# Performance work log

Measured on AMD Instinct MI355X. Metric: run time of the kernel, lower is better.

## Reference

```python
import jax, jax.numpy as jnp
import numpy as np

NUM_HEADS = 8  # from init_kwargs
SR = 2         # sr_ratio from init_kwargs


def layernorm(t, g, b, eps=1e-5):
    mu = jnp.mean(t, axis=-1, keepdims=True)
    var = jnp.mean((t - mu) ** 2, axis=-1, keepdims=True)
    return (t - mu) * jax.lax.rsqrt(var + eps) * g + b


def setup_inputs() -> dict:
    key = jax.random.key(0)
    ks = jax.random.split(key, 6)
    B, C = 4, 256
    Hx = Wx = 64
    Hz = Wz = 32
    N = Hz * Wz + Hx * Wx  # 5120 (template tokens first, then search tokens)
    s = 0.02
    return {
        "x": jax.random.normal(ks[0], (B, N, C), jnp.float32),
        "Wq": jax.random.normal(ks[1], (C, C), jnp.float32) * s,          # nn.Linear(dim, dim, bias=False)
        "Wkv": jax.random.normal(ks[2], (2 * C, C), jnp.float32) * s,     # nn.Linear(dim, 2*dim, bias=False)
        "Wsr": jax.random.normal(ks[3], (C, C, SR, SR), jnp.float32) * s, # Conv2d(dim, dim, k=sr, stride=sr) OIHW
        "bsr": jnp.zeros((C,), jnp.float32),
        "gamma": jnp.ones((C,), jnp.float32),
        "beta": jnp.zeros((C,), jnp.float32),
        "Wproj": jax.random.normal(ks[4], (C, C), jnp.float32) * s,
        "bproj": jnp.zeros((C,), jnp.float32),
        "H_x": Hx, "W_x": Wx, "H_z": Hz, "W_z": Wz,
    }


def reference(x, Wq, Wkv, Wsr, bsr, gamma, beta, Wproj, bproj, H_x, W_x, H_z, W_z):
    B, N, C = x.shape
    h = NUM_HEADS
    d = C // h
    scale = d ** -0.5
    Nz, Nx = H_z * W_z, H_x * W_x

    # q for all tokens: [B, h, N, d]
    q = (x @ Wq.T).reshape(B, N, h, d).transpose(0, 2, 1, 3)

    # spatial reduction (sr_ratio > 1 branch): strided conv + layernorm on each stream
    z_tok, x_tok = x[:, :Nz], x[:, Nz:]
    ker = jnp.transpose(Wsr, (2, 3, 1, 0))  # OIHW -> HWIO

    def sr_branch(t, H, W):
        img = t.reshape(B, H, W, C)  # NHWC; same layout as torch NCHW reshape
        out = jax.lax.conv_general_dilated(
            img, ker, window_strides=(SR, SR), padding="VALID",
            dimension_numbers=("NHWC", "HWIO", "NHWC")) + bsr
        out = out.reshape(B, -1, C)
        return layernorm(out, gamma, beta)

    x_ = sr_branch(x_tok, H_x, W_x)  # [B, (Hx/sr)*(Wx/sr), C]
    z_ = sr_branch(z_tok, H_z, W_z)  # [B, (Hz/sr)*(Wz/sr), C]
    zL = z_.shape[1]
    cat = jnp.concatenate([z_, x_], axis=1)  # [B, L, C]

    kv = (cat @ Wkv.T).reshape(B, -1, 2, h, d).transpose(2, 0, 3, 1, 4)  # [2, B, h, L, d]
    k, v = kv[0], kv[1]

    q_z, q_x = q[:, :, :Nz], q[:, :, Nz:]
    k_z, v_z = k[:, :, :zL], v[:, :, :zL]

    # template queries attend only to reduced template keys/values
    attn_z = jax.nn.softmax(jnp.einsum("bhqd,bhkd->bhqk", q_z, k_z) * scale, axis=-1)
    out_z = jnp.einsum("bhqk,bhkd->bhqd", attn_z, v_z).transpose(0, 2, 1, 3).reshape(B, Nz, C)

    # search queries attend to full (template+search) reduced keys/values
    attn_x = jax.nn.softmax(jnp.einsum("bhqd,bhkd->bhqk", q_x, k) * scale, axis=-1)
    out_x = jnp.einsum("bhqk,bhkd->bhqd", attn_x, v).transpose(0, 2, 1, 3).reshape(B, Nx, C)

    out = jnp.concatenate([out_z, out_x], axis=1)
    return out @ Wproj.T + bproj
```

## Files before the change

kernel.cpp:

```cpp
#include <hip/hip_runtime.h>
#include <hip/hip_bf16.h>
#include <cstddef>

#define BATCH 4
#define CCH 256
#define NHEAD 8
#define DHEAD 32
#define NZ 1024
#define NX 4096
#define NTOK 5120
#define LKV 1280
#define QC 0.25503486f

typedef __attribute__((ext_vector_type(8))) short bf16x8;
typedef __attribute__((ext_vector_type(4))) float floatx4;

__device__ inline short f2bf(float f) {
  __hip_bfloat16 h = __float2bfloat16(f);
  return __builtin_bit_cast(short, h);
}
__device__ inline unsigned int pk2(float a, float b) {
  unsigned int lo = (unsigned short)f2bf(a);
  unsigned int hi = (unsigned short)f2bf(b);
  return lo | (hi << 16);
}
__device__ inline unsigned int pk2f(float a, float b) {
  unsigned int ua = __builtin_bit_cast(unsigned int, a) + 0x8000u;
  unsigned int ub = __builtin_bit_cast(unsigned int, b) + 0x8000u;
  return __builtin_amdgcn_perm(ub, ua, 0x07060302u);
}
__device__ inline void cvt8(const float* __restrict__ src, short* __restrict__ dst, int i) {
  float4 v0 = ((const float4*)src)[i * 2];
  float4 v1 = ((const float4*)src)[i * 2 + 1];
  uint4 u;
  u.x = pk2(v0.x, v0.y); u.y = pk2(v0.z, v0.w);
  u.z = pk2(v1.x, v1.y); u.w = pk2(v1.z, v1.w);
  ((uint4*)dst)[i] = u;
}

__global__ __launch_bounds__(256) void prep_weights(const float* __restrict__ Wq,
                                                    const float* __restrict__ Wkv,
                                                    const float* __restrict__ Wproj,
                                                    const float* __restrict__ Wsr,
                                                    const float* __restrict__ x,
                                                    short* __restrict__ Wqb,
                                                    short* __restrict__ Wkvb,
                                                    short* __restrict__ Wprojb,
                                                    short* __restrict__ Wkb,
                                                    short* __restrict__ xb) {
  int blk = blockIdx.x, tid = threadIdx.x;
  if (blk < 32) {
    cvt8(Wq, Wqb, blk * 256 + tid);
  } else if (blk < 96) {
    cvt8(Wkv, Wkvb, (blk - 32) * 256 + tid);
  } else if (blk < 128) {
    cvt8(Wproj, Wprojb, (blk - 96) * 256 + tid);
  } else if (blk < 1152) {
    int i = (blk - 128) * 256 + tid;
    int co = i >> 10;
    int rem = i & 1023;
    int di = rem >> 9, dj = (rem >> 8) & 1, ci = rem & 255;
    Wkb[i] = f2bf(Wsr[((co * 256 + ci) * 2 + di) * 2 + dj]);
  } else {
    cvt8(x, xb, (blk - 1152) * 256 + tid);
  }
}

#define G64_DECL()                                                           \
  __shared__ short As[64][72];                                               \
  __shared__ short Bs[64][72];                                               \
  int tid = threadIdx.x;                                                     \
  int wave = tid >> 6, lg = (tid & 63) >> 4, lr = tid & 15;                  \
  int sr = tid >> 2, sc = tid & 3;                                           \
  floatx4 acc[4] = {{0.f,0.f,0.f,0.f},{0.f,0.f,0.f,0.f},                     \
                    {0.f,0.f,0.f,0.f},{0.f,0.f,0.f,0.f}};

#define G64_MFMA8()                                                          \
    __syncthreads();                                                         \
    {                                                                        \
      bf16x8 af0 = *(bf16x8*)&As[wave * 16 + lr][lg * 8];                    \
      bf16x8 af1 = *(bf16x8*)&As[wave * 16 + lr][32 + lg * 8];               \
      _Pragma("unroll") for (int n = 0; n < 4; ++n) {                        \
        bf16x8 bf0 = *(bf16x8*)&Bs[n * 16 + lr][lg * 8];                     \
        bf16x8 bf1 = *(bf16x8*)&Bs[n * 16 + lr][32 + lg * 8];                \
        acc[n] = __builtin_amdgcn_mfma_f32_16x16x32_bf16(af0, bf0, acc[n], 0, 0, 0); \
        acc[n] = __builtin_amdgcn_mfma_f32_16x16x32_bf16(af1, bf1, acc[n], 0, 0, 0); \
      }                                                                      \
    }

__global__ __launch_bounds__(256) void gemm_qconv(const short* __restrict__ xb,
                                                  const short* __restrict__ Wqb,
                                                  const short* __restrict__ Wkb,
                                                  short* __restrict__ qbf,
                                                  float* __restrict__ cat_pre) {
  G64_DECL()
  int bidx = blockIdx.x;
  if (bidx < 1280) {
    int bm = (bidx >> 2) * 64, bn = (bidx & 3) * 64;
    for (int k0 = 0; k0 < 256; k0 += 64) {
      bf16x8 a0 = *(const bf16x8*)&xb[(size_t)(bm + sr) * 256 + k0 + sc * 8];
      bf16x8 a1 = *(const bf16x8*)&xb[(size_t)(bm + sr) * 256 + k0 + (sc + 4) * 8];
      bf16x8 b0 = *(const bf16x8*)&Wqb[(size_t)(bn + sr) * 256 + k0 + sc * 8];
      bf16x8 b1 = *(const bf16x8*)&Wqb[(size_t)(bn + sr) * 256 + k0 + (sc + 4) * 8];
      __syncthreads();
      *(bf16x8*)&As[sr][sc * 8] = a0;
      *(bf16x8*)&As[sr][(sc + 4) * 8] = a1;
      *(bf16x8*)&Bs[sr][sc * 8] = b0;
      *(bf16x8*)&Bs[sr][(sc + 4) * 8] = b1;
      G64_MFMA8()
    }
#pragma unroll
    for (int n = 0; n < 4; ++n) {
      int c = bn + 16 * n + lr;
      int h = c >> 5, d = c & 31;
#pragma unroll
      for (int reg = 0; reg < 4; ++reg) {
        int m = bm + wave * 16 + 4 * lg + reg;
        int b = m / NTOK, tok = m - b * NTOK;
        qbf[((size_t)(b * 8 + h) * NTOK + tok) * 32 + d] = f2bf(acc[n][reg] * QC);
      }
    }
  } else {
    int idx = bidx - 1280;
    int mt = idx >> 2;
    int bm = mt * 64, bn = (idx & 3) * 64;
    int bq = mt / 20;
    int tloc = (mt % 20) * 64 + sr;
    for (int k0 = 0; k0 < 1024; k0 += 64) {
      int di = k0 >> 9, dj = (k0 >> 8) & 1;
      int srow;
      if (tloc < 256) {
        int oi = tloc >> 4, oj = tloc & 15;
        srow = bq * NTOK + (2 * oi + di) * 32 + (2 * oj + dj);
      } else {
        int tt = tloc - 256;
        int oi = tt >> 5, oj = tt & 31;
        srow = bq * NTOK + NZ + (2 * oi + di) * 64 + (2 * oj + dj);
      }
      int cb = k0 & 255;
      bf16x8 a0 = *(const bf16x8*)&xb[(size_t)srow * 256 + cb + sc * 8];
      bf16x8 a1 = *(const bf16x8*)&xb[(size_t)srow * 256 + cb + (sc + 4) * 8];
      bf16x8 b0 = *(const bf16x8*)&Wkb[(size_t)(bn + sr) * 1024 + k0 + sc * 8];
      bf16x8 b1 = *(const bf16x8*)&Wkb[(size_t)(bn + sr) * 1024 + k0 + (sc + 4) * 8];
      __syncthreads();
      *(bf16x8*)&As[sr][sc * 8] = a0;
      *(bf16x8*)&As[sr][(sc + 4) * 8] = a1;
      *(bf16x8*)&Bs[sr][sc * 8] = b0;
      *(bf16x8*)&Bs[sr][(sc + 4) * 8] = b1;
      G64_MFMA8()
    }
#pragma unroll
    for (int n = 0; n < 4; ++n) {
      int c = bn + 16 * n + lr;
#pragma unroll
      for (int reg = 0; reg < 4; ++reg) {
        int m = bm + wave * 16 + 4 * lg + reg;
        cat_pre[(size_t)m * 256 + c] = acc[n][reg];
      }
    }
  }
}

__global__ __launch_bounds__(256) void gemm_kv64(const float* __restrict__ cat_pre,
                                                 const float* __restrict__ bsr,
                                                 const float* __restrict__ gamma,
                                                 const float* __restrict__ beta,
                                                 const short* __restrict__ Bm,
                                                 short* __restrict__ Kbf,
                                                 short* __restrict__ Vtb) {
  __shared__ short Af[64][264];
  __shared__ short Bs[64][72];
  int tid = threadIdx.x;
  int wave = tid >> 6, lg = (tid & 63) >> 4, lr = tid & 15;
  int sr = tid >> 2, sc = tid & 3;
  int lane = tid & 63;
  floatx4 acc[4] = {{0.f,0.f,0.f,0.f},{0.f,0.f,0.f,0.f},
                    {0.f,0.f,0.f,0.f},{0.f,0.f,0.f,0.f}};
  int bm = blockIdx.y * 64, bn = blockIdx.x * 64;

  float4 bb = *(const float4*)&bsr[lane * 4];
  float4 g4 = *(const float4*)&gamma[lane * 4];
  float4 be = *(const float4*)&beta[lane * 4];
#pragma unroll
  for (int i = 0; i < 16; ++i) {
    int row = bm + wave * 16 + i;
    float4 v = *(const float4*)&cat_pre[(size_t)row * 256 + lane * 4];
    v.x += bb.x; v.y += bb.y; v.z += bb.z; v.w += bb.w;
    float s = (v.x + v.y) + (v.z + v.w);
#pragma unroll
    for (int mask = 1; mask < 64; mask <<= 1) s += __shfl_xor(s, mask, 64);
    float mu = s * (1.f / 256.f);
    float4 dv;
    dv.x = v.x - mu; dv.y = v.y - mu; dv.z = v.z - mu; dv.w = v.w - mu;
    float q = dv.x * dv.x + dv.y * dv.y + dv.z * dv.z + dv.w * dv.w;
#pragma unroll
    for (int mask = 1; mask < 64; mask <<= 1) q += __shfl_xor(q, mask, 64);
    float rs = rsqrtf(q * (1.f / 256.f) + 1e-5f);
    uint2 st;
    st.x = pk2(dv.x * rs * g4.x + be.x, dv.y * rs * g4.y + be.y);
    st.y = pk2(dv.z * rs * g4.z + be.z, dv.w * rs * g4.w + be.w);
    *(uint2*)&Af[wave * 16 + i][lane * 4] = st;
  }
  __syncthreads();

  for (int k0 = 0; k0 < 256; k0 += 64) {
    bf16x8 b0 = *(const bf16x8*)&Bm[(size_t)(bn + sr) * 256 + k0 + sc * 8];
    bf16x8 b1 = *(const bf16x8*)&Bm[(size_t)(bn + sr) * 256 + k0 + (sc + 4) * 8];
    __syncthreads();
    *(bf16x8*)&Bs[sr][sc * 8] = b0;
    *(bf16x8*)&Bs[sr][(sc + 4) * 8] = b1;
    __syncthreads();
    bf16x8 af0 = *(bf16x8*)&Af[wave * 16 + lr][k0 + lg * 8];
    bf16x8 af1 = *(bf16x8*)&Af[wave * 16 + lr][k0 + 32 + lg * 8];
#pragma unroll
    for (int n = 0; n < 4; ++n) {
      bf16x8 bf0 = *(bf16x8*)&Bs[n * 16 + lr][lg * 8];
      bf16x8 bf1 = *(bf16x8*)&Bs[n * 16 + lr][32 + lg * 8];
      acc[n] = __builtin_amdgcn_mfma_f32_16x16x32_bf16(af0, bf0, acc[n], 0, 0, 0);
      acc[n] = __builtin_amdgcn_mfma_f32_16x16x32_bf16(af1, bf1, acc[n], 0, 0, 0);
    }
  }
#pragma unroll
  for (int n = 0; n < 4; ++n) {
    int c = bn + 16 * n + lr;
#pragma unroll
    for (int reg = 0; reg < 4; ++reg) {
      int m = bm + wave * 16 + 4 * lg + reg;
      int b = m / LKV, kvg = m - b * LKV;
      if (c < 256) {
        int h = c >> 5, d = c & 31;
        Kbf[((size_t)(b * 8 + h) * LKV + kvg) * 32 + d] = f2bf(acc[n][reg]);
      } else {
        int cc = c - 256;
        int h = cc >> 5, d = cc & 31;
        int tile = kvg >> 6, kvin = kvg & 63;
        Vtb[(((size_t)(b * 8 + h) * 20 + tile) * 32 + d) * 64 + kvin] = f2bf(acc[n][reg]);
      }
    }
  }
}

__global__ __launch_bounds__(256) void gemm_proj64(const short* __restrict__ A,
                                                   const short* __restrict__ Bm,
                                                   const float* __restrict__ bias,
                                                   float* __restrict__ Cm) {
  G64_DECL()
  int bm = blockIdx.y * 64, bn = blockIdx.x * 64;
  for (int k0 = 0; k0 < 256; k0 += 64) {
    bf16x8 a0 = *(const bf16x8*)&A[(size_t)(bm + sr) * 256 + k0 + sc * 8];
    bf16x8 a1 = *(const bf16x8*)&A[(size_t)(bm + sr) * 256 + k0 + (sc + 4) * 8];
    bf16x8 b0 = *(const bf16x8*)&Bm[(size_t)(bn + sr) * 256 + k0 + sc * 8];
    bf16x8 b1 = *(const bf16x8*)&Bm[(size_t)(bn + sr) * 256 + k0 + (sc + 4) * 8];
    __syncthreads();
    *(bf16x8*)&As[sr][sc * 8] = a0;
    *(bf16x8*)&As[sr][(sc + 4) * 8] = a1;
    *(bf16x8*)&Bs[sr][sc * 8] = b0;
    *(bf16x8*)&Bs[sr][(sc + 4) * 8] = b1;
    G64_MFMA8()
  }
#pragma unroll
  for (int n = 0; n < 4; ++n) {
    int c = bn + 16 * n + lr;
    float bv = bias[c];
#pragma unroll
    for (int reg = 0; reg < 4; ++reg) {
      int m = bm + wave * 16 + 4 * lg + reg;
      Cm[(size_t)m * 256 + c] = acc[n][reg] + bv;
    }
  }
}

__global__ __launch_bounds__(64) void attn_fused(const short* __restrict__ qbf,
                                                 const short* __restrict__ Kbf,
                                                 const short* __restrict__ Vtb,
                                                 short* __restrict__ attn_out) {
  int orig = blockIdx.x;
  int xcd = orig & 7, s = orig >> 3;
  int bh, q0, kvlen;
  if (s < 256) {
    bh = xcd + 8 * (s >> 6);
    q0 = NZ + (s & 63) * 64;
    kvlen = LKV;
  } else {
    int s2 = s - 256;
    bh = xcd + 8 * (s2 >> 4);
    q0 = (s2 & 15) * 64;
    kvlen = 256;
  }
  int b = bh >> 3, hh = bh & 7;
  int tid = threadIdx.x;
  int lane = tid & 63, lg = lane >> 4, lr = lane & 15;

  __shared__ short Ps[64][72];

  int qtok = q0;
  const short* qb = qbf + ((size_t)bh * NTOK + qtok) * 32;
  bf16x8 qf[4];
#pragma unroll
  for (int qi = 0; qi < 4; ++qi)
    qf[qi] = *(const bf16x8*)&qb[(16 * qi + lr) * 32 + lg * 8];

  const short* Kb = Kbf + (size_t)bh * LKV * 32;
  const short* Vb = Vtb + (size_t)bh * 20 * 2048;

  floatx4 oacc[4][2];
#pragma unroll
  for (int qi = 0; qi < 4; ++qi)
#pragma unroll
    for (int n = 0; n < 2; ++n) oacc[qi][n] = (floatx4){0.f, 0.f, 0.f, 0.f};
  float lsum[4] = {0.f, 0.f, 0.f, 0.f};

  bf16x8 kfc[4], vfc[2][2];
#pragma unroll
  for (int m = 0; m < 4; ++m)
    kfc[m] = *(const bf16x8*)&Kb[(size_t)(16 * m + lr) * 32 + lg * 8];
#pragma unroll
  for (int n = 0; n < 2; ++n)
#pragma unroll
    for (int kb = 0; kb < 2; ++kb)
      vfc[n][kb] = *(const bf16x8*)&Vb[(16 * n + lr) * 64 + kb * 32 + lg * 8];

  for (int l0 = 0; l0 < kvlen; l0 += 64) {
    __builtin_amdgcn_sched_barrier(0);
#pragma unroll
    for (int qi = 0; qi < 4; ++qi) {
      floatx4 st[4];
#pragma unroll
      for (int m = 0; m < 4; ++m)
        st[m] = __builtin_amdgcn_mfma_f32_16x16x32_bf16(
            kfc[m], qf[qi], (floatx4){0.f, 0.f, 0.f, 0.f}, 0, 0, 0);
      int pr = 16 * qi + lr;
#pragma unroll
      for (int m = 0; m < 4; ++m) {
        float p0 = __builtin_amdgcn_exp2f(st[m][0]);
        float p1 = __builtin_amdgcn_exp2f(st[m][1]);
        float p2 = __builtin_amdgcn_exp2f(st[m][2]);
        float p3 = __builtin_amdgcn_exp2f(st[m][3]);
        lsum[qi] += (p0 + p1) + (p2 + p3);
        uint2 w;
        w.x = pk2f(p0, p1);
        w.y = pk2f(p2, p3);
        *(uint2*)&Ps[pr][16 * m + 4 * lg] = w;
      }
    }

    bf16x8 kfn[4], vfn[2][2];
    int l1 = l0 + 64;
    if (l1 < kvlen) {
      const short* Vbt = Vb + (l1 >> 6) * 2048;
#pragma unroll
      for (int m = 0; m < 4; ++m)
        kfn[m] = *(const bf16x8*)&Kb[(size_t)(l1 + 16 * m + lr) * 32 + lg * 8];
#pragma unroll
      for (int n = 0; n < 2; ++n)
#pragma unroll
        for (int kb = 0; kb < 2; ++kb)
          vfn[n][kb] = *(const bf16x8*)&Vbt[(16 * n + lr) * 64 + kb * 32 + lg * 8];
    }

    __builtin_amdgcn_sched_barrier(0);

#pragma unroll
    for (int qi = 0; qi < 4; ++qi)
#pragma unroll
      for (int kb = 0; kb < 2; ++kb) {
        bf16x8 pf = *(bf16x8*)&Ps[16 * qi + lr][kb * 32 + lg * 8];
#pragma unroll
        for (int n = 0; n < 2; ++n)
          oacc[qi][n] = __builtin_amdgcn_mfma_f32_16x16x32_bf16(pf, vfc[n][kb], oacc[qi][n], 0, 0, 0);
      }

#pragma unroll
    for (int m = 0; m < 4; ++m) kfc[m] = kfn[m];
#pragma unroll
    for (int n = 0; n < 2; ++n)
#pragma unroll
      for (int kb = 0; kb < 2; ++kb) vfc[n][kb] = vfn[n][kb];
  }

#pragma unroll
  for (int qi = 0; qi < 4; ++qi) {
    lsum[qi] += __shfl_xor(lsum[qi], 16, 64);
    lsum[qi] += __shfl_xor(lsum[qi], 32, 64);
  }

#pragma unroll
  for (int qi = 0; qi < 4; ++qi)
#pragma unroll
    for (int reg = 0; reg < 4; ++reg) {
      float lv = __shfl(lsum[qi], 4 * lg + reg, 64);
      float inv = 1.f / lv;
      int gr = b * NTOK + qtok + 16 * qi + 4 * lg + reg;
      short* ob = attn_out + (size_t)gr * CCH + hh * DHEAD;
      ob[lr]      = f2bf(oacc[qi][0][reg] * inv);
      ob[16 + lr] = f2bf(oacc[qi][1][reg] * inv);
    }
}

extern "C" void kernel_launch(void* const* d_in, const int* in_sizes, int n_in,
                              void* d_out, int out_size, void* d_ws, size_t ws_size,
                              hipStream_t stream) {
  (void)in_sizes; (void)n_in; (void)out_size; (void)ws_size;
  const float* x     = (const float*)d_in[0];
  const float* Wq    = (const float*)d_in[1];
  const float* Wkv   = (const float*)d_in[2];
  const float* Wsr   = (const float*)d_in[3];
  const float* bsr   = (const float*)d_in[4];
  const float* gamma = (const float*)d_in[5];
  const float* beta  = (const float*)d_in[6];
  const float* Wproj = (const float*)d_in[7];
  const float* bproj = (const float*)d_in[8];
  float* out = (float*)d_out;
  float* ws  = (float*)d_ws;

  short* qbf      = (short*)ws;
  short* attn_out = (short*)(ws + 2621440);
  float* cat_pre  = ws + 7864320;
  short* Kbf      = (short*)(ws + 9830400);
  short* Vtb      = (short*)(ws + 10485760);
  short* Wqb      = (short*)(ws + 11141120);
  short* Wkvb     = (short*)(ws + 11173888);
  short* Wkb      = (short*)(ws + 11239424);
  short* Wprojb   = (short*)(ws + 11370496);
  short* xb       = attn_out;

  prep_weights<<<3712, 256, 0, stream>>>(Wq, Wkv, Wproj, Wsr, x, Wqb, Wkvb, Wprojb, Wkb, xb);
  gemm_qconv<<<1600, 256, 0, stream>>>(xb, Wqb, Wkb, qbf, cat_pre);
  gemm_kv64<<<dim3(8, 80), 256, 0, stream>>>(cat_pre, bsr, gamma, beta, Wkvb, Kbf, Vtb);
  attn_fused<<<2560, 64, 0, stream>>>(qbf, Kbf, Vtb, attn_out);
  gemm_proj64<<<dim3(4, 320), 256, 0, stream>>>(attn_out, Wprojb, bproj, out);
}
```

Baseline: 190.8 us.

## Widen conv/Q GEMM tiles to full 256 columns and fuse layernorm into conv epilogue

The combined Q/conv GEMM now has each block compute a full 64x256 output tile instead of 64x64, so the grid shrinks from 1600 to 400 blocks and the A tile is loaded once per row block rather than four times. Because a conv block now holds complete 256-channel rows, bias and layernorm run in its epilogue and the result is written as bf16, so the KV GEMM no longer reads an fp32 intermediate or normalizes it. The trade-off is four times more accumulator registers and LDS per block, which lowers occupancy. Only 80 conv blocks now do the long K=1024 loop, which may leave those blocks on the critical path.

```diff
diff --git a/kernel.cpp b/kernel.cpp
--- a/kernel.cpp
+++ b/kernel.cpp
@@ -91,41 +91,28 @@
 __global__ __launch_bounds__(256) void gemm_qconv(const short* __restrict__ xb,
                                                   const short* __restrict__ Wqb,
                                                   const short* __restrict__ Wkb,
+                                                  const float* __restrict__ bsr,
+                                                  const float* __restrict__ gamma,
+                                                  const float* __restrict__ beta,
                                                   short* __restrict__ qbf,
-                                                  float* __restrict__ cat_pre) {
-  G64_DECL()
+                                                  short* __restrict__ catb) {
+  __shared__ short As[64][72];
+  __shared__ short Bs[4][64][72];
+  int tid = threadIdx.x;
+  int wave = tid >> 6, lg = (tid & 63) >> 4, lr = tid & 15;
+  int sr = tid >> 2, sc = tid & 3;
+  floatx4 acc[4][4];
+#pragma unroll
+  for (int nb = 0; nb < 4; ++nb)
+#pragma unroll
+    for (int n = 0; n < 4; ++n) acc[nb][n] = (floatx4){0.f, 0.f, 0.f, 0.f};
+
   int bidx = blockIdx.x;
-  if (bidx < 1280) {
-    int bm = (bidx >> 2) * 64, bn = (bidx & 3) * 64;
-    for (int k0 = 0; k0 < 256; k0 += 64) {
-      bf16x8 a0 = *(const bf16x8*)&xb[(size_t)(bm + sr) * 256 + k0 + sc * 8];
-      bf16x8 a1 = *(const bf16x8*)&xb[(size_t)(bm + sr) * 256 + k0 + (sc + 4) * 8];
-      bf16x8 b0 = *(const bf16x8*)&Wqb[(size_t)(bn + sr) * 256 + k0 + sc * 8];
-      bf16x8 b1 = *(const bf16x8*)&Wqb[(size_t)(bn + sr) * 256 + k0 + (sc + 4) * 8];
-      __syncthreads();
-      *(bf16x8*)&As[sr][sc * 8] = a0;
-      *(bf16x8*)&As[sr][(sc + 4) * 8] = a1;
-      *(bf16x8*)&Bs[sr][sc * 8] = b0;
-      *(bf16x8*)&Bs[sr][(sc + 4) * 8] = b1;
-      G64_MFMA8()
-    }
-#pragma unroll
-    for (int n = 0; n < 4; ++n) {
-      int c = bn + 16 * n + lr;
-      int h = c >> 5, d = c & 31;
-#pragma unroll
-      for (int reg = 0; reg < 4; ++reg) {
-        int m = bm + wave * 16 + 4 * lg + reg;
-        int b = m / NTOK, tok = m - b * NTOK;
-        qbf[((size_t)(b * 8 + h) * NTOK + tok) * 32 + d] = f2bf(acc[n][reg] * QC);
-      }
-    }
-  } else {
-    int idx = bidx - 1280;
-    int mt = idx >> 2;
-    int bm = mt * 64, bn = (idx & 3) * 64;
+  if (bidx < 80) {
+    int mt = bidx;
     int bq = mt / 20;
     int tloc = (mt % 20) * 64 + sr;
+    int rowbase = mt * 64;
     for (int k0 = 0; k0 < 1024; k0 += 64) {
       int di = k0 >> 9, dj = (k0 >> 8) & 1;
       int srow;
@@ -140,85 +127,130 @@
       int cb = k0 & 255;
       bf16x8 a0 = *(const bf16x8*)&xb[(size_t)srow * 256 + cb + sc * 8];
       bf16x8 a1 = *(const bf16x8*)&xb[(size_t)srow * 256 + cb + (sc + 4) * 8];
-      bf16x8 b0 = *(const bf16x8*)&Wkb[(size_t)(bn + sr) * 1024 + k0 + sc * 8];
-      bf16x8 b1 = *(const bf16x8*)&Wkb[(size_t)(bn + sr) * 1024 + k0 + (sc + 4) * 8];
+      bf16x8 br[4][2];
+#pragma unroll
+      for (int nb = 0; nb < 4; ++nb) {
+        br[nb][0] = *(const bf16x8*)&Wkb[(size_t)(nb * 64 + sr) * 1024 + k0 + sc * 8];
+        br[nb][1] = *(const bf16x8*)&Wkb[(size_t)(nb * 64 + sr) * 1024 + k0 + (sc + 4) * 8];
+      }
       __syncthreads();
       *(bf16x8*)&As[sr][sc * 8] = a0;
       *(bf16x8*)&As[sr][(sc + 4) * 8] = a1;
-      *(bf16x8*)&Bs[sr][sc * 8] = b0;
-      *(bf16x8*)&Bs[sr][(sc + 4) * 8] = b1;
-      G64_MFMA8()
-    }
-#pragma unroll
-    for (int n = 0; n < 4; ++n) {
-      int c = bn + 16 * n + lr;
-#pragma unroll
-      for (int reg = 0; reg < 4; ++reg) {
-        int m = bm + wave * 16 + 4 * lg + reg;
-        cat_pre[(size_t)m * 256 + c] = acc[n][reg];
-      }
-    }
-  }
-}
-
-__global__ __launch_bounds__(256) void gemm_kv64(const float* __restrict__ cat_pre,
-                                                 const float* __restrict__ bsr,
-                                                 const float* __restrict__ gamma,
-                                                 const float* __restrict__ beta,
+#pragma unroll
+      for (int nb = 0; nb < 4; ++nb) {
+        *(bf16x8*)&Bs[nb][sr][sc * 8] = br[nb][0];
+        *(bf16x8*)&Bs[nb][sr][(sc + 4) * 8] = br[nb][1];
+      }
+      __syncthreads();
+      bf16x8 af0 = *(bf16x8*)&As[wave * 16 + lr][lg * 8];
+      bf16x8 af1 = *(bf16x8*)&As[wave * 16 + lr][32 + lg * 8];
+#pragma unroll
+      for (int nb = 0; nb < 4; ++nb)
+#pragma unroll
+        for (int n = 0; n < 4; ++n) {
+          bf16x8 bf0 = *(bf16x8*)&Bs[nb][n * 16 + lr][lg * 8];
+          bf16x8 bf1 = *(bf16x8*)&Bs[nb][n * 16 + lr][32 + lg * 8];
+          acc[nb][n] = __builtin_amdgcn_mfma_f32_16x16x32_bf16(af0, bf0, acc[nb][n], 0, 0, 0);
+          acc[nb][n] = __builtin_amdgcn_mfma_f32_16x16x32_bf16(af1, bf1, acc[nb][n], 0, 0, 0);
+        }
+    }
+#pragma unroll
+    for (int reg = 0; reg < 4; ++reg) {
+      int rrow = rowbase + wave * 16 + 4 * lg + reg;
+      float v[16];
+      float s = 0.f;
+#pragma unroll
+      for (int nb = 0; nb < 4; ++nb)
+#pragma unroll
+        for (int n = 0; n < 4; ++n) {
+          int c = nb * 64 + 16 * n + lr;
+          float t = acc[nb][n][reg] + bsr[c];
+          v[nb * 4 + n] = t;
+          s += t;
+        }
+#pragma unroll
+      for (int mask = 1; mask < 16; mask <<= 1) s += __shfl_xor(s, mask, 64);
+      float mu = s * (1.f / 256.f);
+      float q = 0.f;
+#pragma unroll
+      for (int i = 0; i < 16; ++i) { float d = v[i] - mu; q += d * d; }
+#pragma unroll
+      for (int mask = 1; mask < 16; mask <<= 1) q += __shfl_xor(q, mask, 64);
+      float rs = rsqrtf(q * (1.f / 256.f) + 1e-5f);
+#pragma unroll
+      for (int nb = 0; nb < 4; ++nb)
+#pragma unroll
+        for (int n = 0; n < 4; ++n) {
+          int c = nb * 64 + 16 * n + lr;
+          catb[(size_t)rrow * 256 + c] = f2bf((v[nb * 4 + n] - mu) * rs * gamma[c] + beta[c]);
+        }
+    }
+  } else {
+    int qi = bidx - 80;
+    int bm = qi * 64;
+    for (int k0 = 0; k0 < 256; k0 += 64) {
+      bf16x8 a0 = *(const bf16x8*)&xb[(size_t)(bm + sr) * 256 + k0 + sc * 8];
+      bf16x8 a1 = *(const bf16x8*)&xb[(size_t)(bm + sr) * 256 + k0 + (sc + 4) * 8];
+      bf16x8 br[4][2];
+#pragma unroll
+      for (int nb = 0; nb < 4; ++nb) {
+        br[nb][0] = *(const bf16x8*)&Wqb[(size_t)(nb * 64 + sr) * 256 + k0 + sc * 8];
+        br[nb][1] = *(const bf16x8*)&Wqb[(size_t)(nb * 64 + sr) * 256 + k0 + (sc + 4) * 8];
+      }
+      __syncthreads();
+      *(bf16x8*)&As[sr][sc * 8] = a0;
+      *(bf16x8*)&As[sr][(sc + 4) * 8] = a1;
+#pragma unroll
+      for (int nb = 0; nb < 4; ++nb) {
+        *(bf16x8*)&Bs[nb][sr][sc * 8] = br[nb][0];
+        *(bf16x8*)&Bs[nb][sr][(sc + 4) * 8] = br[nb][1];
+      }
+      __syncthreads();
+      bf16x8 af0 = *(bf16x8*)&As[wave * 16 + lr][lg * 8];
+      bf16x8 af1 = *(bf16x8*)&As[wave * 16 + lr][32 + lg * 8];
+#pragma unroll
+      for (int nb = 0; nb < 4; ++nb)
+#pragma unroll
+        for (int n = 0; n < 4; ++n) {
+          bf16x8 bf0 = *(bf16x8*)&Bs[nb][n * 16 + lr][lg * 8];
+          bf16x8 bf1 = *(bf16x8*)&Bs[nb][n * 16 + lr][32 + lg * 8];
+          acc[nb][n] = __builtin_amdgcn_mfma_f32_16x16x32_bf16(af0, bf0, acc[nb][n], 0, 0, 0);
+          acc[nb][n] = __builtin_amdgcn_mfma_f32_16x16x32_bf16(af1, bf1, acc[nb][n], 0, 0, 0);
+        }
+    }
+#pragma unroll
+    for (int nb = 0; nb < 4; ++nb)
+#pragma unroll
+      for (int n = 0; n < 4; ++n) {
+        int c = nb * 64 + 16 * n + lr;
+        int h = c >> 5, d = c & 31;
+#pragma unroll
+        for (int reg = 0; reg < 4; ++reg) {
+          int m = bm + wave * 16 + 4 * lg + reg;
+          int b = m / NTOK, tok = m - b * NTOK;
+          qbf[((size_t)(b * 8 + h) * NTOK + tok) * 32 + d] = f2bf(acc[nb][n][reg] * QC);
+        }
+      }
+  }
+}
+
+__global__ __launch_bounds__(256) void gemm_kv64(const short* __restrict__ A,
                                                  const short* __restrict__ Bm,
                                                  short* __restrict__ Kbf,
                                                  short* __restrict__ Vtb) {
-  __shared__ short Af[64][264];
-  __shared__ short Bs[64][72];
-  int tid = threadIdx.x;
-  int wave = tid >> 6, lg = (tid & 63) >> 4, lr = tid & 15;
-  int sr = tid >> 2, sc = tid & 3;
-  int lane = tid & 63;
-  floatx4 acc[4] = {{0.f,0.f,0.f,0.f},{0.f,0.f,0.f,0.f},
-                    {0.f,0.f,0.f,0.f},{0.f,0.f,0.f,0.f}};
+  G64_DECL()
   int bm = blockIdx.y * 64, bn = blockIdx.x * 64;
-
-  float4 bb = *(const float4*)&bsr[lane * 4];
-  float4 g4 = *(const float4*)&gamma[lane * 4];
-  float4 be = *(const float4*)&beta[lane * 4];
-#pragma unroll
-  for (int i = 0; i < 16; ++i) {
-    int row = bm + wave * 16 + i;
-    float4 v = *(const float4*)&cat_pre[(size_t)row * 256 + lane * 4];
-    v.x += bb.x; v.y += bb.y; v.z += bb.z; v.w += bb.w;
-    float s = (v.x + v.y) + (v.z + v.w);
-#pragma unroll
-    for (int mask = 1; mask < 64; mask <<= 1) s += __shfl_xor(s, mask, 64);
-    float mu = s * (1.f / 256.f);
-    float4 dv;
-    dv.x = v.x - mu; dv.y = v.y - mu; dv.z = v.z - mu; dv.w = v.w - mu;
-    float q = dv.x * dv.x + dv.y * dv.y + dv.z * dv.z + dv.w * dv.w;
-#pragma unroll
-    for (int mask = 1; mask < 64; mask <<= 1) q += __shfl_xor(q, mask, 64);
-    float rs = rsqrtf(q * (1.f / 256.f) + 1e-5f);
-    uint2 st;
-    st.x = pk2(dv.x * rs * g4.x + be.x, dv.y * rs * g4.y + be.y);
-    st.y = pk2(dv.z * rs * g4.z + be.z, dv.w * rs * g4.w + be.w);
-    *(uint2*)&Af[wave * 16 + i][lane * 4] = st;
-  }
-  __syncthreads();
-
   for (int k0 = 0; k0 < 256; k0 += 64) {
+    bf16x8 a0 = *(const bf16x8*)&A[(size_t)(bm + sr) * 256 + k0 + sc * 8];
+    bf16x8 a1 = *(const bf16x8*)&A[(size_t)(bm + sr) * 256 + k0 + (sc + 4) * 8];
     bf16x8 b0 = *(const bf16x8*)&Bm[(size_t)(bn + sr) * 256 + k0 + sc * 8];
     bf16x8 b1 = *(const bf16x8*)&Bm[(size_t)(bn + sr) * 256 + k0 + (sc + 4) * 8];
     __syncthreads();
+    *(bf16x8*)&As[sr][sc * 8] = a0;
+    *(bf16x8*)&As[sr][(sc + 4) * 8] = a1;
     *(bf16x8*)&Bs[sr][sc * 8] = b0;
     *(bf16x8*)&Bs[sr][(sc + 4) * 8] = b1;
-    __syncthreads();
-    bf16x8 af0 = *(bf16x8*)&Af[wave * 16 + lr][k0 + lg * 8];
-    bf16x8 af1 = *(bf16x8*)&Af[wave * 16 + lr][k0 + 32 + lg * 8];
-#pragma unroll
-    for (int n = 0; n < 4; ++n) {
-      bf16x8 bf0 = *(bf16x8*)&Bs[n * 16 + lr][lg * 8];
-      bf16x8 bf1 = *(bf16x8*)&Bs[n * 16 + lr][32 + lg * 8];
-      acc[n] = __builtin_amdgcn_mfma_f32_16x16x32_bf16(af0, bf0, acc[n], 0, 0, 0);
-      acc[n] = __builtin_amdgcn_mfma_f32_16x16x32_bf16(af1, bf1, acc[n], 0, 0, 0);
-    }
+    G64_MFMA8()
   }
 #pragma unroll
   for (int n = 0; n < 4; ++n) {
@@ -415,7 +447,7 @@
 
   short* qbf      = (short*)ws;
   short* attn_out = (short*)(ws + 2621440);
-  float* cat_pre  = ws + 7864320;
+  short* catb     = (short*)(ws + 9175040);
   short* Kbf      = (short*)(ws + 9830400);
   short* Vtb      = (short*)(ws + 10485760);
   short* Wqb      = (short*)(ws + 11141120);
@@ -425,8 +457,8 @@
   short* xb       = attn_out;
 
   prep_weights<<<3712, 256, 0, stream>>>(Wq, Wkv, Wproj, Wsr, x, Wqb, Wkvb, Wprojb, Wkb, xb);
-  gemm_qconv<<<1600, 256, 0, stream>>>(xb, Wqb, Wkb, qbf, cat_pre);
-  gemm_kv64<<<dim3(8, 80), 256, 0, stream>>>(cat_pre, bsr, gamma, beta, Wkvb, Kbf, Vtb);
+  gemm_qconv<<<400, 256, 0, stream>>>(xb, Wqb, Wkb, bsr, gamma, beta, qbf, catb);
+  gemm_kv64<<<dim3(8, 80), 256, 0, stream>>>(catb, Wkvb, Kbf, Vtb);
   attn_fused<<<2560, 64, 0, stream>>>(qbf, Kbf, Vtb, attn_out);
   gemm_proj64<<<dim3(4, 320), 256, 0, stream>>>(attn_out, Wprojb, bproj, out);
 }
```

After: 187.6 us. No clear change (-1.7%).
